# Kernel tuning notes

Hardware: AMD Instinct MI355X
Metric: run time of the kernel (lower is better)

The kernel has to match this reference:

```python
import jax, jax.numpy as jnp
import numpy as np

N = 50000      # nodes (atoms)
E = 1000000    # edges (bonds within cutoff)
L = 3          # num_interactions
G = 512        # graphs in batch
H = 128        # hidden_channels == num_filters
NGAUSS = 50    # num_gaussians
CUTOFF = 10.0
ZMAX = 100     # atomic numbers, < num_embeddings=120
LOG2 = float(np.log(2.0))


def ssp(x):
    # ShiftedSoftplus: softplus(x) - log(2)
    return jax.nn.softplus(x) - LOG2


def setup_inputs() -> dict:
    key = jax.random.key(0)
    ks = jax.random.split(key, 16)

    def w(k, shape, fan_in):
        return jax.random.normal(k, shape, jnp.float32) / np.sqrt(fan_in)

    z = jax.random.randint(ks[0], (N,), 1, ZMAX)
    edge_src = jax.random.randint(ks[1], (E,), 0, N)
    edge_dst = jax.random.randint(ks[2], (E,), 0, N)
    batch = jnp.sort(jax.random.randint(ks[3], (N,), 0, G))
    edge_weight = jax.random.uniform(ks[4], (E,), jnp.float32) * CUTOFF  # distances in [0, cutoff)
    edge_attr = jax.random.normal(ks[5], (E, NGAUSS), jnp.float32)       # gaussian-smeared distances
    return {
        'z': z, 'edge_src': edge_src, 'edge_dst': edge_dst, 'batch': batch,
        'num_graphs': G,
        'edge_weight': edge_weight, 'edge_attr': edge_attr,
        'emb': w(ks[6], (120, H), 1.0),
        'mlp_w1': w(ks[7], (L, NGAUSS, H), NGAUSS), 'mlp_b1': jnp.zeros((L, H), jnp.float32),
        'mlp_w2': w(ks[8], (L, H, H), H), 'mlp_b2': jnp.zeros((L, H), jnp.float32),
        'cf_w1': w(ks[9], (L, H, H), H),
        'cf_w2': w(ks[10], (L, H, H), H), 'cf_b2': jnp.zeros((L, H), jnp.float32),
        'lin_w': w(ks[11], (L, H, H), H), 'lin_b': jnp.zeros((L, H), jnp.float32),
        'ro_w1': w(ks[12], (H, 5 * H), H), 'ro_b1': jnp.zeros((5 * H,), jnp.float32),
        'ro_w2': w(ks[13], (5 * H, H), 5 * H), 'ro_b2': jnp.zeros((H,), jnp.float32),
        'ro_w3': w(ks[14], (H, 1), H), 'ro_b3': jnp.zeros((1,), jnp.float32),
    }


def reference(z, edge_src, edge_dst, batch, num_graphs, edge_weight, edge_attr,
              emb, mlp_w1, mlp_b1, mlp_w2, mlp_b2, cf_w1, cf_w2, cf_b2,
              lin_w, lin_b, ro_w1, ro_b1, ro_w2, ro_b2, ro_w3, ro_b3):
    n_nodes = z.shape[0]
    # simple_z=True: h = relu(Embedding(z))
    h = jax.nn.relu(emb[z])                                   # [N, H]
    # cosine cutoff on distances (shared across blocks)
    C = 0.5 * (jnp.cos(edge_weight * jnp.pi / CUTOFF) + 1.0)  # [E]
    for l in range(L):
        # SchNet filter network on edge attributes
        Wf = ssp(edge_attr @ mlp_w1[l] + mlp_b1[l]) @ mlp_w2[l] + mlp_b2[l]
        Wf = Wf * C[:, None]                                  # [E, H]
        x = h @ cf_w1[l]                                      # CFConv.lin1 (no bias)
        msg = x[edge_src] * Wf                                # gather + filter modulation
        agg = jax.ops.segment_sum(msg, edge_dst, num_segments=n_nodes)  # scatter-add
        x = agg @ cf_w2[l] + cf_b2[l]                         # CFConv.lin2
        x = ssp(x) @ lin_w[l] + lin_b[l]                      # act + block linear
        h = h + x                                             # residual from model forward
    # ReadOutLayer
    hh = ssp(h @ ro_w1 + ro_b1)                               # [N, 5H]
    pooled = jax.ops.segment_sum(hh, batch, num_segments=num_graphs)  # segment_csr 'add'
    out = ssp(pooled @ ro_w2 + ro_b2) @ ro_w3 + ro_b3         # [G, 1]
    return out
```

## Files before the change

### kernel.cpp

```cpp
#include <hip/hip_runtime.h>
#include <math.h>

#define N_NODES 50000
#define N_EDGES 1000000
#define LAYERS  3
#define G_GRAPHS 512
#define H 128
#define NG 50
#define PI_F 3.14159265358979323846f
#define LOG2_F 0.6931471805599453f

typedef __attribute__((ext_vector_type(4))) float f32x4;
typedef __attribute__((ext_vector_type(8))) short short8;

__device__ __forceinline__ float ssp(float v) {
    float t = __expf(-fabsf(v));
    return fmaxf(v, 0.0f) + __logf(1.0f + t) - LOG2_F;
}

__device__ __forceinline__ unsigned short f2bf(float f) {
    unsigned u = __float_as_uint(f);
    unsigned r = (u + 0x7fff + ((u >> 16) & 1)) >> 16;
    return (unsigned short)r;
}
__device__ __forceinline__ float bf2f(unsigned short h) {
    return __uint_as_float((unsigned)h << 16);
}

__global__ __launch_bounds__(256) void init_h(const int* __restrict__ z,
                                              const float* __restrict__ emb,
                                              float* __restrict__ h) {
    int idx = blockIdx.x * 256 + threadIdx.x;
    if (idx >= N_NODES * (H / 4)) return;
    int n = idx >> 5;
    int c4 = idx & 31;
    int zv = z[n];
    float4 v = *(const float4*)(emb + (size_t)zv * H + c4 * 4);
    v.x = fmaxf(v.x, 0.f); v.y = fmaxf(v.y, 0.f);
    v.z = fmaxf(v.z, 0.f); v.w = fmaxf(v.w, 0.f);
    *(float4*)(h + (size_t)n * H + c4 * 4) = v;
}

__global__ __launch_bounds__(256) void hist_kernel(const int* __restrict__ edst,
                                                   int* __restrict__ cnt) {
    int e = blockIdx.x * 256 + threadIdx.x;
    if (e < N_EDGES) atomicAdd(&cnt[edst[e]], 1);
}

__global__ __launch_bounds__(1024) void scan_kernel(const int* __restrict__ cnt,
                                                    int* __restrict__ cur) {
    __shared__ int wsum[16];
    __shared__ int carry_s;
    int tid = threadIdx.x;
    int wid = tid >> 6, lane = tid & 63;
    if (tid == 0) carry_s = 0;
    __syncthreads();
    for (int base = 0; base < N_NODES; base += 1024) {
        int i = base + tid;
        int v = (i < N_NODES) ? cnt[i] : 0;
        int s = v;
#pragma unroll
        for (int d = 1; d < 64; d <<= 1) {
            int t = __shfl_up(s, d, 64);
            if (lane >= d) s += t;
        }
        if (lane == 63) wsum[wid] = s;
        __syncthreads();
        if (wid == 0) {
            int ws = (lane < 16) ? wsum[lane] : 0;
#pragma unroll
            for (int d = 1; d < 16; d <<= 1) {
                int t = __shfl_up(ws, d, 64);
                if (lane >= d) ws += t;
            }
            if (lane < 16) wsum[lane] = ws;
        }
        __syncthreads();
        int waveoff = (wid > 0) ? wsum[wid - 1] : 0;
        int carry = carry_s;
        if (i < N_NODES) cur[i] = carry + waveoff + s - v;
        __syncthreads();
        if (tid == 1023) carry_s = carry + wsum[15];
    }
}

__global__ __launch_bounds__(256) void scatter_kernel(const int* __restrict__ edst,
                                                      int* __restrict__ cur,
                                                      int* __restrict__ perm) {
    int e = blockIdx.x * 256 + threadIdx.x;
    if (e < N_EDGES) {
        int p = atomicAdd(&cur[edst[e]], 1);
        perm[p] = e;
    }
}

__global__ __launch_bounds__(256) void prep_idx(const int* __restrict__ perm,
                                                const int* __restrict__ esrc,
                                                const int* __restrict__ edst,
                                                const float* __restrict__ ew,
                                                int* __restrict__ Sp,
                                                int* __restrict__ Dp,
                                                float* __restrict__ Cp) {
    int pos = blockIdx.x * 256 + threadIdx.x;
    if (pos >= N_EDGES) return;
    int ge = perm[pos];
    Sp[pos] = esrc[ge];
    Dp[pos] = edst[ge];
    Cp[pos] = 0.5f * (cosf(ew[ge] * (PI_F / 10.0f)) + 1.0f);
}

__global__ __launch_bounds__(256) void prep_attr(const int* __restrict__ perm,
                                                 const float* __restrict__ eattr,
                                                 unsigned short* __restrict__ pattr) {
    int t = blockIdx.x * 256 + threadIdx.x;
    int pos = t >> 3, kq = t & 7;
    if (pos >= N_EDGES) return;
    int ge = perm[pos];
    int k0 = kq * 8;
    float v[8] = {0.f, 0.f, 0.f, 0.f, 0.f, 0.f, 0.f, 0.f};
    const float* row = eattr + (size_t)ge * NG;
    if (k0 + 8 <= NG) {
#pragma unroll
        for (int q = 0; q < 4; ++q) {
            float2 a = *(const float2*)(row + k0 + 2 * q);
            v[2 * q] = a.x; v[2 * q + 1] = a.y;
        }
    } else if (k0 < NG) {
        float2 a = *(const float2*)(row + k0);
        v[0] = a.x; v[1] = a.y;
    }
    uint4 wv;
    wv.x = (unsigned)f2bf(v[0]) | ((unsigned)f2bf(v[1]) << 16);
    wv.y = (unsigned)f2bf(v[2]) | ((unsigned)f2bf(v[3]) << 16);
    wv.z = (unsigned)f2bf(v[4]) | ((unsigned)f2bf(v[5]) << 16);
    wv.w = (unsigned)f2bf(v[6]) | ((unsigned)f2bf(v[7]) << 16);
    *(uint4*)(pattr + (size_t)pos * 64 + k0) = wv;
}

__global__ __launch_bounds__(256) void conv_w(const float* __restrict__ mlp_w1,
                                              const float* __restrict__ mlp_w2,
                                              unsigned short* __restrict__ w1t,
                                              unsigned short* __restrict__ w2t) {
    int idx = blockIdx.x * 256 + threadIdx.x;
    const int n1 = LAYERS * 128 * 64;
    if (idx < n1) {
        int l = idx / (128 * 64);
        int rem = idx - l * 128 * 64;
        int col = rem >> 6, k = rem & 63;
        float v = (k < NG) ? mlp_w1[(size_t)l * NG * H + (size_t)k * H + col] : 0.f;
        w1t[idx] = f2bf(v);
        return;
    }
    int idx2 = idx - n1;
    if (idx2 < LAYERS * 128 * 128) {
        int l = idx2 / (128 * 128);
        int rem = idx2 - l * 128 * 128;
        int col = rem >> 7, k = rem & 127;
        w2t[idx2] = f2bf(mlp_w2[(size_t)l * H * H + (size_t)k * H + col]);
    }
}

__global__ __launch_bounds__(256) void conv_nodew(const float* __restrict__ src,
                                                  unsigned short* __restrict__ hi,
                                                  unsigned short* __restrict__ lo,
                                                  int ncols) {
    int idx = blockIdx.x * 256 + threadIdx.x;
    if (idx >= ncols * 128) return;
    int col = idx >> 7, k = idx & 127;
    float v = src[(size_t)k * ncols + col];
    unsigned short h16 = f2bf(v);
    hi[idx] = h16;
    lo[idx] = f2bf(v - bf2f(h16));
}

#define F_BIAS 1
#define F_POOL 8

template <int FLAGS>
__global__ __launch_bounds__(256, 4) void node_gemm_mfma(const float* __restrict__ A,
                                                         const unsigned short* __restrict__ BtHi,
                                                         const unsigned short* __restrict__ BtLo,
                                                         const float* __restrict__ bias,
                                                         float* __restrict__ Out,
                                                         const int* __restrict__ batch,
                                                         int nRows, int NC) {
    __shared__ __align__(16) char ldsHi[64 * 256];
    __shared__ __align__(16) char ldsLo[64 * 256];
    int tid = threadIdx.x;
    int rowBase = blockIdx.x * 64;
    int colOff = blockIdx.y * 128;
    int rlim = nRows - rowBase; if (rlim > 64) rlim = 64;

    for (int idx = tid; idx < 64 * 32; idx += 256) {
        int r = idx >> 5, q = idx & 31;
        float4 v = make_float4(0.f, 0.f, 0.f, 0.f);
        if (r < rlim) v = *(const float4*)(A + (size_t)(rowBase + r) * H + q * 4);
        unsigned short h0 = f2bf(v.x), h1 = f2bf(v.y), h2 = f2bf(v.z), h3 = f2bf(v.w);
        unsigned short l0 = f2bf(v.x - bf2f(h0)), l1 = f2bf(v.y - bf2f(h1));
        unsigned short l2 = f2bf(v.z - bf2f(h2)), l3 = f2bf(v.w - bf2f(h3));
        int byte = (r << 8) + (q << 3);
        byte ^= (r & 7) << 4;
        *(uint2*)(ldsHi + byte) = make_uint2((unsigned)h0 | ((unsigned)h1 << 16),
                                             (unsigned)h2 | ((unsigned)h3 << 16));
        *(uint2*)(ldsLo + byte) = make_uint2((unsigned)l0 | ((unsigned)l1 << 16),
                                             (unsigned)l2 | ((unsigned)l3 << 16));
    }
    __syncthreads();

    int w = tid >> 6, lane = tid & 63;
    int lg = lane >> 4, cg = lane & 15;
    int swA = (cg & 7) << 4;

    f32x4 acc[4][2];
#pragma unroll
    for (int n = 0; n < 2; ++n) {
        float b = (FLAGS & F_BIAS) ? bias[colOff + w * 32 + n * 16 + cg] : 0.f;
        f32x4 t = {b, b, b, b};
#pragma unroll
        for (int m = 0; m < 4; ++m) acc[m][n] = t;
    }

#pragma unroll
    for (int kc = 0; kc < 4; ++kc) {
        short8 aHi[4], aLo[4], bHi[2], bLo[2];
#pragma unroll
        for (int m = 0; m < 4; ++m) {
            int byte = ((m * 16 + cg) << 8) + ((kc * 32 + lg * 8) << 1);
            aHi[m] = *(short8*)(ldsHi + (byte ^ swA));
            aLo[m] = *(short8*)(ldsLo + (byte ^ swA));
        }
#pragma unroll
        for (int n = 0; n < 2; ++n) {
            size_t off = (size_t)(colOff + w * 32 + n * 16 + cg) * 128 + kc * 32 + lg * 8;
            bHi[n] = *(const short8*)(BtHi + off);
            bLo[n] = *(const short8*)(BtLo + off);
        }
#pragma unroll
        for (int m = 0; m < 4; ++m)
#pragma unroll
            for (int n = 0; n < 2; ++n) {
                acc[m][n] = __builtin_amdgcn_mfma_f32_16x16x32_bf16(aHi[m], bHi[n], acc[m][n], 0, 0, 0);
                acc[m][n] = __builtin_amdgcn_mfma_f32_16x16x32_bf16(aLo[m], bHi[n], acc[m][n], 0, 0, 0);
                acc[m][n] = __builtin_amdgcn_mfma_f32_16x16x32_bf16(aHi[m], bLo[n], acc[m][n], 0, 0, 0);
            }
    }

    if (FLAGS & F_POOL) {
        int cur = -1;
        float s[2] = {0.f, 0.f};
#pragma unroll
        for (int m = 0; m < 4; ++m) {
#pragma unroll
            for (int i = 0; i < 4; ++i) {
                int row = m * 16 + lg * 4 + i;
                int b = (row < rlim) ? batch[rowBase + row] : -1;
                if (b != cur) {
                    if (cur >= 0) {
#pragma unroll
                        for (int n = 0; n < 2; ++n)
                            unsafeAtomicAdd(Out + (size_t)cur * NC + colOff + w * 32 + n * 16 + cg, s[n]);
                    }
                    cur = b;
                    s[0] = 0.f; s[1] = 0.f;
                }
                if (b >= 0) {
#pragma unroll
                    for (int n = 0; n < 2; ++n) s[n] += ssp(acc[m][n][i]);
                }
            }
        }
        if (cur >= 0) {
#pragma unroll
            for (int n = 0; n < 2; ++n)
                unsafeAtomicAdd(Out + (size_t)cur * NC + colOff + w * 32 + n * 16 + cg, s[n]);
        }
    } else {
#pragma unroll
        for (int m = 0; m < 4; ++m)
#pragma unroll
            for (int i = 0; i < 4; ++i) {
                int row = m * 16 + lg * 4 + i;
                if (row < rlim) {
#pragma unroll
                    for (int n = 0; n < 2; ++n)
                        Out[(size_t)(rowBase + row) * NC + colOff + w * 32 + n * 16 + cg] = acc[m][n][i];
                }
            }
    }
}

__global__ __launch_bounds__(256, 4) void node_gemm2_mfma(const float* __restrict__ Agg,
                                                          const unsigned short* __restrict__ W2hi,
                                                          const unsigned short* __restrict__ W2lo,
                                                          const float* __restrict__ b2,
                                                          const unsigned short* __restrict__ WLhi,
                                                          const unsigned short* __restrict__ WLlo,
                                                          const float* __restrict__ bl,
                                                          float* __restrict__ Hio,
                                                          int nRows) {
    __shared__ __align__(16) char ldsHi[64 * 256];
    __shared__ __align__(16) char ldsLo[64 * 256];
    int tid = threadIdx.x;
    int rowBase = blockIdx.x * 64;
    int rlim = nRows - rowBase; if (rlim > 64) rlim = 64;

    for (int idx = tid; idx < 64 * 32; idx += 256) {
        int r = idx >> 5, q = idx & 31;
        float4 v = make_float4(0.f, 0.f, 0.f, 0.f);
        if (r < rlim) v = *(const float4*)(Agg + (size_t)(rowBase + r) * H + q * 4);
        unsigned short h0 = f2bf(v.x), h1 = f2bf(v.y), h2 = f2bf(v.z), h3 = f2bf(v.w);
        unsigned short l0 = f2bf(v.x - bf2f(h0)), l1 = f2bf(v.y - bf2f(h1));
        unsigned short l2 = f2bf(v.z - bf2f(h2)), l3 = f2bf(v.w - bf2f(h3));
        int byte = (r << 8) + (q << 3);
        byte ^= (r & 7) << 4;
        *(uint2*)(ldsHi + byte) = make_uint2((unsigned)h0 | ((unsigned)h1 << 16),
                                             (unsigned)h2 | ((unsigned)h3 << 16));
        *(uint2*)(ldsLo + byte) = make_uint2((unsigned)l0 | ((unsigned)l1 << 16),
                                             (unsigned)l2 | ((unsigned)l3 << 16));
    }
    __syncthreads();

    int w = tid >> 6, lane = tid & 63;
    int lg = lane >> 4, cg = lane & 15;
    int swA = (cg & 7) << 4;

    f32x4 acc[4][2];
#pragma unroll
    for (int n = 0; n < 2; ++n) {
        float b = b2[w * 32 + n * 16 + cg];
        f32x4 t = {b, b, b, b};
#pragma unroll
        for (int m = 0; m < 4; ++m) acc[m][n] = t;
    }
#pragma unroll
    for (int kc = 0; kc < 4; ++kc) {
        short8 aHi[4], aLo[4], bHi[2], bLo[2];
#pragma unroll
        for (int m = 0; m < 4; ++m) {
            int byte = ((m * 16 + cg) << 8) + ((kc * 32 + lg * 8) << 1);
            aHi[m] = *(short8*)(ldsHi + (byte ^ swA));
            aLo[m] = *(short8*)(ldsLo + (byte ^ swA));
        }
#pragma unroll
        for (int n = 0; n < 2; ++n) {
            size_t off = (size_t)(w * 32 + n * 16 + cg) * 128 + kc * 32 + lg * 8;
            bHi[n] = *(const short8*)(W2hi + off);
            bLo[n] = *(const short8*)(W2lo + off);
        }
#pragma unroll
        for (int m = 0; m < 4; ++m)
#pragma unroll
            for (int n = 0; n < 2; ++n) {
                acc[m][n] = __builtin_amdgcn_mfma_f32_16x16x32_bf16(aHi[m], bHi[n], acc[m][n], 0, 0, 0);
                acc[m][n] = __builtin_amdgcn_mfma_f32_16x16x32_bf16(aLo[m], bHi[n], acc[m][n], 0, 0, 0);
                acc[m][n] = __builtin_amdgcn_mfma_f32_16x16x32_bf16(aHi[m], bLo[n], acc[m][n], 0, 0, 0);
            }
    }
    __syncthreads();

#pragma unroll
    for (int m = 0; m < 4; ++m)
#pragma unroll
        for (int n = 0; n < 2; ++n)
#pragma unroll
            for (int i = 0; i < 4; ++i) {
                int row = m * 16 + lg * 4 + i;
                int col = w * 32 + n * 16 + cg;
                float v = ssp(acc[m][n][i]);
                unsigned short hh = f2bf(v);
                unsigned short ll = f2bf(v - bf2f(hh));
                int byte = (row << 8) + (col << 1);
                byte ^= (row & 7) << 4;
                *(unsigned short*)(ldsHi + byte) = hh;
                *(unsigned short*)(ldsLo + byte) = ll;
            }
    __syncthreads();

    f32x4 acc2[4][2];
#pragma unroll
    for (int n = 0; n < 2; ++n) {
        float b = bl[w * 32 + n * 16 + cg];
        f32x4 t = {b, b, b, b};
#pragma unroll
        for (int m = 0; m < 4; ++m) acc2[m][n] = t;
    }
#pragma unroll
    for (int kc = 0; kc < 4; ++kc) {
        short8 aHi[4], aLo[4], bHi[2], bLo[2];
#pragma unroll
        for (int m = 0; m < 4; ++m) {
            int byte = ((m * 16 + cg) << 8) + ((kc * 32 + lg * 8) << 1);
            aHi[m] = *(short8*)(ldsHi + (byte ^ swA));
            aLo[m] = *(short8*)(ldsLo + (byte ^ swA));
        }
#pragma unroll
        for (int n = 0; n < 2; ++n) {
            size_t off = (size_t)(w * 32 + n * 16 + cg) * 128 + kc * 32 + lg * 8;
            bHi[n] = *(const short8*)(WLhi + off);
            bLo[n] = *(const short8*)(WLlo + off);
        }
#pragma unroll
        for (int m = 0; m < 4; ++m)
#pragma unroll
            for (int n = 0; n < 2; ++n) {
                acc2[m][n] = __builtin_amdgcn_mfma_f32_16x16x32_bf16(aHi[m], bHi[n], acc2[m][n], 0, 0, 0);
                acc2[m][n] = __builtin_amdgcn_mfma_f32_16x16x32_bf16(aLo[m], bHi[n], acc2[m][n], 0, 0, 0);
                acc2[m][n] = __builtin_amdgcn_mfma_f32_16x16x32_bf16(aHi[m], bLo[n], acc2[m][n], 0, 0, 0);
            }
    }

#pragma unroll
    for (int m = 0; m < 4; ++m)
#pragma unroll
        for (int i = 0; i < 4; ++i) {
            int row = m * 16 + lg * 4 + i;
            if (row < rlim) {
#pragma unroll
                for (int n = 0; n < 2; ++n) {
                    float* p = Hio + (size_t)(rowBase + row) * H + w * 32 + n * 16 + cg;
                    *p += acc2[m][n][i];
                }
            }
        }
}

template <bool IDXP, bool ATTRP>
__global__ __launch_bounds__(256, 5) void edge_kernel(
        const unsigned short* __restrict__ pattr,
        const float* __restrict__ eattr,
        const int* __restrict__ perm,
        const int* __restrict__ esrc,
        const int* __restrict__ edst,
        const float* __restrict__ ew,
        const int* __restrict__ Sp,
        const int* __restrict__ Dp,
        const float* __restrict__ Cp,
        const unsigned short* __restrict__ W1t,
        const float* __restrict__ b1,
        const unsigned short* __restrict__ W2t,
        const float* __restrict__ b2,
        const float* __restrict__ x,
        float* __restrict__ agg) {
    __shared__ __align__(16) char lds[28832];
    float* accT = (float*)(lds + 24576);
    int* RunDst = (int*)(lds + 28800);

    int tid = threadIdx.x;
    int e0 = blockIdx.x * 64;
    int w = tid >> 6, lane = tid & 63;

    for (int i = tid; i < 8 * 132; i += 256) accT[i] = 0.f;

    int ge = 0;
    if (!ATTRP || !IDXP) ge = perm[e0 + lane];
    int S, D; float C;
    if (IDXP) {
        S = Sp[e0 + lane]; D = Dp[e0 + lane]; C = Cp[e0 + lane];
    } else {
        S = esrc[ge]; D = edst[ge];
        C = 0.5f * (cosf(ew[ge] * (PI_F / 10.0f)) + 1.0f);
    }
    int prevd = -1, nextd = -1;
    if (e0 > 0)            prevd = IDXP ? Dp[e0 - 1]  : edst[perm[e0 - 1]];
    if (e0 + 64 < N_EDGES) nextd = IDXP ? Dp[e0 + 64] : edst[perm[e0 + 64]];

    if (ATTRP) {
#pragma unroll
        for (int half = 0; half < 2; ++half) {
            int idx2 = lane + half * 64;
            int row = w * 16 + (idx2 >> 3);
            int q = idx2 & 7;
            uint4 v = *(const uint4*)(pattr + (((size_t)(e0 + row)) << 6) + q * 8);
            int byte = (row << 7) + (q << 4);
            byte ^= (row & 7) << 4;
            *(uint4*)(lds + byte) = v;
        }
    } else {
        int row = w * 16 + (lane >> 2);
        int grow = __shfl(ge, row);
        int jbase = (lane & 3) * 8;
#pragma unroll
        for (int j = 0; j < 8; ++j) {
            int k2 = jbase + j;
            float a0 = 0.f, a1 = 0.f;
            if (k2 < 25) {
                float2 t = *(const float2*)(eattr + (size_t)grow * NG + 2 * k2);
                a0 = t.x; a1 = t.y;
            }
            unsigned p = (unsigned)f2bf(a0) | ((unsigned)f2bf(a1) << 16);
            int byte = (row << 7) + (k2 << 2);
            byte ^= (row & 7) << 4;
            *(unsigned*)(lds + byte) = p;
        }
    }

    int lg = lane >> 4, cg = lane & 15;
    int eB = w * 16 + cg;
    int swz = (eB & 7) << 4;
    int le0 = w * 16 + lg * 4;

    f32x4 acc1[8];
#pragma unroll
    for (int mt = 0; mt < 8; ++mt)
        acc1[mt] = *(const f32x4*)(b1 + mt * 16 + lg * 4);
#pragma unroll
    for (int kc = 0; kc < 2; ++kc) {
        int byteB = (eB << 7) + (kc << 6) + (lg << 4);
        short8 bfrag = *(short8*)(lds + (byteB ^ swz));
#pragma unroll
        for (int mt = 0; mt < 8; ++mt) {
            short8 afrag = *(const short8*)(W1t + ((mt * 16 + cg) << 6) + (kc << 5) + (lg << 3));
            acc1[mt] = __builtin_amdgcn_mfma_f32_16x16x32_bf16(afrag, bfrag, acc1[mt], 0, 0, 0);
        }
    }
#pragma unroll
    for (int mt = 0; mt < 8; ++mt) {
        f32x4 v = acc1[mt];
        unsigned p0 = (unsigned)f2bf(ssp(v[0])) | ((unsigned)f2bf(ssp(v[1])) << 16);
        unsigned p1 = (unsigned)f2bf(ssp(v[2])) | ((unsigned)f2bf(ssp(v[3])) << 16);
        int byte = 8192 + (eB << 8) + (mt << 5) + (lg << 3);
        *(uint2*)(lds + (byte ^ swz)) = make_uint2(p0, p1);
    }

    f32x4 acc2[8];
#pragma unroll
    for (int n = 0; n < 8; ++n) {
        float bb = b2[n * 16 + cg];
        f32x4 t = {bb, bb, bb, bb};
        acc2[n] = t;
    }
#pragma unroll
    for (int kc = 0; kc < 4; ++kc) {
        int byteA = 8192 + (eB << 8) + (kc << 6) + (lg << 4);
        short8 afrag = *(short8*)(lds + (byteA ^ swz));
#pragma unroll
        for (int n = 0; n < 8; ++n) {
            short8 bfrag = *(const short8*)(W2t + ((n * 16 + cg) << 7) + (kc << 5) + (lg << 3));
            acc2[n] = __builtin_amdgcn_mfma_f32_16x16x32_bf16(afrag, bfrag, acc2[n], 0, 0, 0);
        }
    }

    float xv[4][8];
#pragma unroll
    for (int i = 0; i < 4; ++i) {
        int sle = __shfl(S, le0 + i);
        const float* xrow = x + (size_t)sle * H + cg;
#pragma unroll
        for (int n = 0; n < 8; ++n) xv[i][n] = xrow[n * 16];
    }

    int dprev = __shfl_up(D, 1, 64);
    int flag = (lane > 0 && D != dprev) ? 1 : 0;
    int rid = flag;
#pragma unroll
    for (int s2 = 1; s2 < 64; s2 <<= 1) {
        int o = __shfl_up(rid, s2, 64);
        if (lane >= s2) rid += o;
    }
    int nruns = __shfl(rid, 63) + 1;
    if (w == 0 && (lane == 0 || flag) && rid < 8) RunDst[rid] = D;

    asm volatile("s_waitcnt lgkmcnt(0)" ::: "memory");
    __builtin_amdgcn_s_barrier();
    asm volatile("" ::: "memory");

    int curR = -1, curD = 0;
    float part[8];
#pragma unroll
    for (int i = 0; i < 4; ++i) {
        int le = le0 + i;
        int r  = __shfl(rid, le);
        int dd = __shfl(D, le);
        float cf = __shfl(C, le);
        float m[8];
#pragma unroll
        for (int n = 0; n < 8; ++n) m[n] = xv[i][n] * acc2[n][i] * cf;
        if (r != curR) {
            if (curR >= 0) {
                if (curR < 8) {
#pragma unroll
                    for (int n = 0; n < 8; ++n)
                        atomicAdd(accT + curR * 132 + n * 16 + cg, part[n]);
                } else {
#pragma unroll
                    for (int n = 0; n < 8; ++n)
                        unsafeAtomicAdd(agg + (size_t)curD * H + n * 16 + cg, part[n]);
                }
            }
            curR = r; curD = dd;
#pragma unroll
            for (int n = 0; n < 8; ++n) part[n] = m[n];
        } else {
#pragma unroll
            for (int n = 0; n < 8; ++n) part[n] += m[n];
        }
    }
    if (curR < 8) {
#pragma unroll
        for (int n = 0; n < 8; ++n)
            atomicAdd(accT + curR * 132 + n * 16 + cg, part[n]);
    } else {
#pragma unroll
        for (int n = 0; n < 8; ++n)
            unsafeAtomicAdd(agg + (size_t)curD * H + n * 16 + cg, part[n]);
    }

    asm volatile("s_waitcnt lgkmcnt(0)" ::: "memory");
    __builtin_amdgcn_s_barrier();
    asm volatile("" ::: "memory");

    int nstore = (nruns < 8) ? nruns : 8;
    for (int idx = tid; idx < nstore * H; idx += 256) {
        int r = idx >> 7, c = idx & 127;
        float v = accT[r * 132 + c];
        int d = RunDst[r];
        bool shared_run = (r == 0 && d == prevd) || (r == nruns - 1 && d == nextd);
        float* p = agg + (size_t)d * H + c;
        if (shared_run) unsafeAtomicAdd(p, v);
        else *p = v;
    }
}

__global__ __launch_bounds__(128) void final_out(const float* __restrict__ pooled,
                                                 const float* __restrict__ ro_w2,
                                                 const float* __restrict__ ro_b2,
                                                 const float* __restrict__ ro_w3,
                                                 const float* __restrict__ ro_b3,
                                                 float* __restrict__ out) {
    int g = blockIdx.x;
    int c = threadIdx.x;
    float acc = ro_b2[c];
    const float* pr = pooled + (size_t)g * (5 * H);
    for (int k = 0; k < 5 * H; ++k) acc = fmaf(pr[k], ro_w2[(size_t)k * H + c], acc);
    float v = ssp(acc) * ro_w3[c];
    __shared__ float red[128];
    red[c] = v;
    __syncthreads();
    for (int s = 64; s > 0; s >>= 1) {
        if (c < s) red[c] += red[c + s];
        __syncthreads();
    }
    if (c == 0) out[g] = red[0] + ro_b3[0];
}

extern "C" void kernel_launch(void* const* d_in, const int* in_sizes, int n_in,
                              void* d_out, int out_size, void* d_ws, size_t ws_size,
                              hipStream_t stream) {
    const int* z     = (const int*)d_in[0];
    const int* esrc  = (const int*)d_in[1];
    const int* edst  = (const int*)d_in[2];
    const int* batch = (const int*)d_in[3];
    const float* ew    = (const float*)d_in[5];
    const float* eattr = (const float*)d_in[6];
    const float* emb   = (const float*)d_in[7];
    const float* mlp_w1 = (const float*)d_in[8];
    const float* mlp_b1 = (const float*)d_in[9];
    const float* mlp_w2 = (const float*)d_in[10];
    const float* mlp_b2 = (const float*)d_in[11];
    const float* cf_w1  = (const float*)d_in[12];
    const float* cf_w2  = (const float*)d_in[13];
    const float* cf_b2  = (const float*)d_in[14];
    const float* lin_w  = (const float*)d_in[15];
    const float* lin_b  = (const float*)d_in[16];
    const float* ro_w1  = (const float*)d_in[17];
    const float* ro_b1  = (const float*)d_in[18];
    const float* ro_w2  = (const float*)d_in[19];
    const float* ro_b2  = (const float*)d_in[20];
    const float* ro_w3  = (const float*)d_in[21];
    const float* ro_b3  = (const float*)d_in[22];
    float* out = (float*)d_out;

    char* wp = (char*)d_ws;
    auto alloc = [&](size_t bytes) {
        char* p = wp;
        wp += (bytes + 255) & ~(size_t)255;
        return p;
    };
    float* h      = (float*)alloc((size_t)N_NODES * H * 4);
    float* x      = (float*)alloc((size_t)N_NODES * H * 4);
    float* agg    = (float*)alloc((size_t)N_NODES * H * 4);
    float* pooled = (float*)alloc((size_t)G_GRAPHS * 5 * H * 4);
    int*   cnt    = (int*)alloc(N_NODES * 4);
    int*   cur    = (int*)alloc(N_NODES * 4);
    int*   perm   = (int*)alloc((size_t)N_EDGES * 4);
    unsigned short* w1t  = (unsigned short*)alloc((size_t)LAYERS * 128 * 64 * 2);
    unsigned short* w2t  = (unsigned short*)alloc((size_t)LAYERS * 128 * 128 * 2);
    unsigned short* nwhi = (unsigned short*)alloc((size_t)(9 * 16384 + 640 * 128) * 2);
    unsigned short* nwlo = (unsigned short*)alloc((size_t)(9 * 16384 + 640 * 128) * 2);
    int*   Sp = (int*)alloc((size_t)N_EDGES * 4);
    int*   Dp = (int*)alloc((size_t)N_EDGES * 4);
    float* Cp = (float*)alloc((size_t)N_EDGES * 4);
    size_t used_idx = (size_t)(wp - (char*)d_ws);
    unsigned short* pattr = (unsigned short*)alloc((size_t)N_EDGES * 64 * 2);
    size_t used_attr = (size_t)(wp - (char*)d_ws);

    bool idxp  = ws_size >= used_idx;
    bool attrp = ws_size >= used_attr;

    init_h<<<(N_NODES * (H / 4) + 255) / 256, 256, 0, stream>>>(z, emb, h);

    conv_w<<<(LAYERS * 128 * 64 + LAYERS * 128 * 128 + 255) / 256, 256, 0, stream>>>(
        mlp_w1, mlp_w2, w1t, w2t);
    for (int l = 0; l < LAYERS; ++l) {
        conv_nodew<<<(128 * 128 + 255) / 256, 256, 0, stream>>>(
            cf_w1 + (size_t)l * H * H, nwhi + (size_t)l * 16384, nwlo + (size_t)l * 16384, 128);
        conv_nodew<<<(128 * 128 + 255) / 256, 256, 0, stream>>>(
            cf_w2 + (size_t)l * H * H, nwhi + (size_t)(3 + l) * 16384, nwlo + (size_t)(3 + l) * 16384, 128);
        conv_nodew<<<(128 * 128 + 255) / 256, 256, 0, stream>>>(
            lin_w + (size_t)l * H * H, nwhi + (size_t)(6 + l) * 16384, nwlo + (size_t)(6 + l) * 16384, 128);
    }
    conv_nodew<<<(640 * 128 + 255) / 256, 256, 0, stream>>>(
        ro_w1, nwhi + (size_t)9 * 16384, nwlo + (size_t)9 * 16384, 640);

    hipMemsetAsync(cnt, 0, N_NODES * sizeof(int), stream);
    hist_kernel<<<(N_EDGES + 255) / 256, 256, 0, stream>>>(edst, cnt);
    scan_kernel<<<1, 1024, 0, stream>>>(cnt, cur);
    scatter_kernel<<<(N_EDGES + 255) / 256, 256, 0, stream>>>(edst, cur, perm);

    if (idxp)
        prep_idx<<<(N_EDGES + 255) / 256, 256, 0, stream>>>(perm, esrc, edst, ew, Sp, Dp, Cp);
    if (attrp)
        prep_attr<<<(N_EDGES * 8 + 255) / 256, 256, 0, stream>>>(perm, eattr, pattr);

    int rowTiles = (N_NODES + 63) / 64;
    for (int l = 0; l < LAYERS; ++l) {
        node_gemm_mfma<0><<<dim3(rowTiles, 1), 256, 0, stream>>>(
            h, nwhi + (size_t)l * 16384, nwlo + (size_t)l * 16384, nullptr, x, nullptr, N_NODES, H);
        hipMemsetAsync(agg, 0, (size_t)N_NODES * H * sizeof(float), stream);
        if (attrp)
            edge_kernel<true, true><<<N_EDGES / 64, 256, 0, stream>>>(
                pattr, eattr, perm, esrc, edst, ew, Sp, Dp, Cp,
                w1t + (size_t)l * 128 * 64, mlp_b1 + (size_t)l * H,
                w2t + (size_t)l * 128 * 128, mlp_b2 + (size_t)l * H, x, agg);
        else if (idxp)
            edge_kernel<true, false><<<N_EDGES / 64, 256, 0, stream>>>(
                pattr, eattr, perm, esrc, edst, ew, Sp, Dp, Cp,
                w1t + (size_t)l * 128 * 64, mlp_b1 + (size_t)l * H,
                w2t + (size_t)l * 128 * 128, mlp_b2 + (size_t)l * H, x, agg);
        else
            edge_kernel<false, false><<<N_EDGES / 64, 256, 0, stream>>>(
                pattr, eattr, perm, esrc, edst, ew, Sp, Dp, Cp,
                w1t + (size_t)l * 128 * 64, mlp_b1 + (size_t)l * H,
                w2t + (size_t)l * 128 * 128, mlp_b2 + (size_t)l * H, x, agg);
        node_gemm2_mfma<<<dim3(rowTiles, 1), 256, 0, stream>>>(
            agg,
            nwhi + (size_t)(3 + l) * 16384, nwlo + (size_t)(3 + l) * 16384, cf_b2 + (size_t)l * H,
            nwhi + (size_t)(6 + l) * 16384, nwlo + (size_t)(6 + l) * 16384, lin_b + (size_t)l * H,
            h, N_NODES);
    }

    hipMemsetAsync(pooled, 0, (size_t)G_GRAPHS * 5 * H * sizeof(float), stream);
    node_gemm_mfma<F_BIAS | F_POOL><<<dim3(rowTiles, 5), 256, 0, stream>>>(
        h, nwhi + (size_t)9 * 16384, nwlo + (size_t)9 * 16384, ro_b1, pooled, batch, N_NODES, 5 * H);
    final_out<<<G_GRAPHS, 128, 0, stream>>>(pooled, ro_w2, ro_b2, ro_w3, ro_b3, out);
}
```

Measured before the change: 2.027 ms.

## Fuse node GEMMs across layers, embedding init, agg zeroing; shrink edge LDS

Several independent changes land together. The embedding lookup and ReLU are folded into the first lin1 GEMM. The next layer's lin1 GEMM is fused into the tail of node_gemm2, which also zeroes agg in place of a separate memset. The weight-conversion launches are merged into one kernel. The edge kernel's filter-network MLP is restructured into two halves to halve its intermediate LDS buffer, cutting LDS use and run capacity so more blocks fit per CU (launch bound raised to 8). This trades extra register pressure and serialisation in node_gemm2, and a smaller run cache in the edge kernel, for fewer launches and less memory traffic.

```diff
diff --git a/kernel.cpp b/kernel.cpp
--- a/kernel.cpp
+++ b/kernel.cpp
@@ -25,20 +25,6 @@
 }
 __device__ __forceinline__ float bf2f(unsigned short h) {
     return __uint_as_float((unsigned)h << 16);
-}
-
-__global__ __launch_bounds__(256) void init_h(const int* __restrict__ z,
-                                              const float* __restrict__ emb,
-                                              float* __restrict__ h) {
-    int idx = blockIdx.x * 256 + threadIdx.x;
-    if (idx >= N_NODES * (H / 4)) return;
-    int n = idx >> 5;
-    int c4 = idx & 31;
-    int zv = z[n];
-    float4 v = *(const float4*)(emb + (size_t)zv * H + c4 * 4);
-    v.x = fmaxf(v.x, 0.f); v.y = fmaxf(v.y, 0.f);
-    v.z = fmaxf(v.z, 0.f); v.w = fmaxf(v.w, 0.f);
-    *(float4*)(h + (size_t)n * H + c4 * 4) = v;
 }
 
 __global__ __launch_bounds__(256) void hist_kernel(const int* __restrict__ edst,
@@ -160,21 +146,37 @@
     }
 }
 
-__global__ __launch_bounds__(256) void conv_nodew(const float* __restrict__ src,
-                                                  unsigned short* __restrict__ hi,
-                                                  unsigned short* __restrict__ lo,
-                                                  int ncols) {
+__global__ __launch_bounds__(256) void conv_nodew_all(const float* __restrict__ cf_w1,
+                                                      const float* __restrict__ cf_w2,
+                                                      const float* __restrict__ lin_w,
+                                                      const float* __restrict__ ro_w1,
+                                                      unsigned short* __restrict__ hi,
+                                                      unsigned short* __restrict__ lo) {
     int idx = blockIdx.x * 256 + threadIdx.x;
-    if (idx >= ncols * 128) return;
-    int col = idx >> 7, k = idx & 127;
-    float v = src[(size_t)k * ncols + col];
+    const int SQ = LAYERS * 128 * 128;
+    float v; int dst;
+    if (idx < 3 * SQ) {
+        int fam = idx / SQ, rem = idx - fam * SQ;
+        int l = rem / 16384, r2 = rem & 16383;
+        int col = r2 >> 7, k = r2 & 127;
+        const float* src = (fam == 0) ? cf_w1 : ((fam == 1) ? cf_w2 : lin_w);
+        v = src[(size_t)l * 16384 + (size_t)k * 128 + col];
+        dst = (fam * 3 + l) * 16384 + r2;
+    } else {
+        int j = idx - 3 * SQ;
+        if (j >= 640 * 128) return;
+        int col = j >> 7, k = j & 127;
+        v = ro_w1[(size_t)k * 640 + col];
+        dst = 3 * SQ + j;
+    }
     unsigned short h16 = f2bf(v);
-    hi[idx] = h16;
-    lo[idx] = f2bf(v - bf2f(h16));
+    hi[dst] = h16;
+    lo[dst] = f2bf(v - bf2f(h16));
 }
 
 #define F_BIAS 1
 #define F_POOL 8
+#define F_EMB  16
 
 template <int FLAGS>
 __global__ __launch_bounds__(256, 4) void node_gemm_mfma(const float* __restrict__ A,
@@ -183,7 +185,10 @@
                                                          const float* __restrict__ bias,
                                                          float* __restrict__ Out,
                                                          const int* __restrict__ batch,
-                                                         int nRows, int NC) {
+                                                         int nRows, int NC,
+                                                         const int* __restrict__ z,
+                                                         const float* __restrict__ emb,
+                                                         float* __restrict__ hOut) {
     __shared__ __align__(16) char ldsHi[64 * 256];
     __shared__ __align__(16) char ldsLo[64 * 256];
     int tid = threadIdx.x;
@@ -194,7 +199,17 @@
     for (int idx = tid; idx < 64 * 32; idx += 256) {
         int r = idx >> 5, q = idx & 31;
         float4 v = make_float4(0.f, 0.f, 0.f, 0.f);
-        if (r < rlim) v = *(const float4*)(A + (size_t)(rowBase + r) * H + q * 4);
+        if (r < rlim) {
+            if (FLAGS & F_EMB) {
+                int zr = z[rowBase + r];
+                v = *(const float4*)(emb + (size_t)zr * H + q * 4);
+                v.x = fmaxf(v.x, 0.f); v.y = fmaxf(v.y, 0.f);
+                v.z = fmaxf(v.z, 0.f); v.w = fmaxf(v.w, 0.f);
+                *(float4*)(hOut + (size_t)(rowBase + r) * H + q * 4) = v;
+            } else {
+                v = *(const float4*)(A + (size_t)(rowBase + r) * H + q * 4);
+            }
+        }
         unsigned short h0 = f2bf(v.x), h1 = f2bf(v.y), h2 = f2bf(v.z), h3 = f2bf(v.w);
         unsigned short l0 = f2bf(v.x - bf2f(h0)), l1 = f2bf(v.y - bf2f(h1));
         unsigned short l2 = f2bf(v.z - bf2f(h2)), l3 = f2bf(v.w - bf2f(h3));
@@ -289,14 +304,18 @@
     }
 }
 
-__global__ __launch_bounds__(256, 4) void node_gemm2_mfma(const float* __restrict__ Agg,
+template <bool XNEXT>
+__global__ __launch_bounds__(256, 4) void node_gemm2_mfma(float* __restrict__ Agg,
                                                           const unsigned short* __restrict__ W2hi,
                                                           const unsigned short* __restrict__ W2lo,
                                                           const float* __restrict__ b2,
                                                           const unsigned short* __restrict__ WLhi,
                                                           const unsigned short* __restrict__ WLlo,
                                                           const float* __restrict__ bl,
+                                                          const unsigned short* __restrict__ W1nhi,
+                                                          const unsigned short* __restrict__ W1nlo,
                                                           float* __restrict__ Hio,
+                                                          float* __restrict__ xout,
                                                           int nRows) {
     __shared__ __align__(16) char ldsHi[64 * 256];
     __shared__ __align__(16) char ldsLo[64 * 256];
@@ -307,7 +326,11 @@
     for (int idx = tid; idx < 64 * 32; idx += 256) {
         int r = idx >> 5, q = idx & 31;
         float4 v = make_float4(0.f, 0.f, 0.f, 0.f);
-        if (r < rlim) v = *(const float4*)(Agg + (size_t)(rowBase + r) * H + q * 4);
+        if (r < rlim) {
+            float* p = Agg + (size_t)(rowBase + r) * H + q * 4;
+            v = *(float4*)p;
+            *(float4*)p = make_float4(0.f, 0.f, 0.f, 0.f);
+        }
         unsigned short h0 = f2bf(v.x), h1 = f2bf(v.y), h2 = f2bf(v.z), h3 = f2bf(v.w);
         unsigned short l0 = f2bf(v.x - bf2f(h0)), l1 = f2bf(v.y - bf2f(h1));
         unsigned short l2 = f2bf(v.z - bf2f(h2)), l3 = f2bf(v.w - bf2f(h3));
@@ -409,23 +432,93 @@
             }
     }
 
-#pragma unroll
-    for (int m = 0; m < 4; ++m)
-#pragma unroll
-        for (int i = 0; i < 4; ++i) {
-            int row = m * 16 + lg * 4 + i;
-            if (row < rlim) {
+    if (XNEXT) {
+        __syncthreads();
+#pragma unroll
+        for (int m = 0; m < 4; ++m)
+#pragma unroll
+            for (int n = 0; n < 2; ++n)
+#pragma unroll
+                for (int i = 0; i < 4; ++i) {
+                    int row = m * 16 + lg * 4 + i;
+                    int col = w * 32 + n * 16 + cg;
+                    float hnew = 0.f;
+                    if (row < rlim) {
+                        float* p = Hio + (size_t)(rowBase + row) * H + col;
+                        hnew = *p + acc2[m][n][i];
+                        *p = hnew;
+                    }
+                    unsigned short hh = f2bf(hnew);
+                    unsigned short ll = f2bf(hnew - bf2f(hh));
+                    int byte = (row << 8) + (col << 1);
+                    byte ^= (row & 7) << 4;
+                    *(unsigned short*)(ldsHi + byte) = hh;
+                    *(unsigned short*)(ldsLo + byte) = ll;
+                }
+        __syncthreads();
+
+        f32x4 acc3[4][2];
+#pragma unroll
+        for (int n = 0; n < 2; ++n) {
+            f32x4 t = {0.f, 0.f, 0.f, 0.f};
+#pragma unroll
+            for (int m = 0; m < 4; ++m) acc3[m][n] = t;
+        }
+#pragma unroll
+        for (int kc = 0; kc < 4; ++kc) {
+            short8 aHi[4], aLo[4], bHi[2], bLo[2];
+#pragma unroll
+            for (int m = 0; m < 4; ++m) {
+                int byte = ((m * 16 + cg) << 8) + ((kc * 32 + lg * 8) << 1);
+                aHi[m] = *(short8*)(ldsHi + (byte ^ swA));
+                aLo[m] = *(short8*)(ldsLo + (byte ^ swA));
+            }
+#pragma unroll
+            for (int n = 0; n < 2; ++n) {
+                size_t off = (size_t)(w * 32 + n * 16 + cg) * 128 + kc * 32 + lg * 8;
+                bHi[n] = *(const short8*)(W1nhi + off);
+                bLo[n] = *(const short8*)(W1nlo + off);
+            }
+#pragma unroll
+            for (int m = 0; m < 4; ++m)
 #pragma unroll
                 for (int n = 0; n < 2; ++n) {
-                    float* p = Hio + (size_t)(rowBase + row) * H + w * 32 + n * 16 + cg;
-                    *p += acc2[m][n][i];
+                    acc3[m][n] = __builtin_amdgcn_mfma_f32_16x16x32_bf16(aHi[m], bHi[n], acc3[m][n], 0, 0, 0);
+                    acc3[m][n] = __builtin_amdgcn_mfma_f32_16x16x32_bf16(aLo[m], bHi[n], acc3[m][n], 0, 0, 0);
+                    acc3[m][n] = __builtin_amdgcn_mfma_f32_16x16x32_bf16(aHi[m], bLo[n], acc3[m][n], 0, 0, 0);
                 }
-            }
-        }
-}
-
+        }
+#pragma unroll
+        for (int m = 0; m < 4; ++m)
+#pragma unroll
+            for (int i = 0; i < 4; ++i) {
+                int row = m * 16 + lg * 4 + i;
+                if (row < rlim) {
+#pragma unroll
+                    for (int n = 0; n < 2; ++n)
+                        xout[(size_t)(rowBase + row) * H + w * 32 + n * 16 + cg] = acc3[m][n][i];
+                }
+            }
+    } else {
+#pragma unroll
+        for (int m = 0; m < 4; ++m)
+#pragma unroll
+            for (int i = 0; i < 4; ++i) {
+                int row = m * 16 + lg * 4 + i;
+                if (row < rlim) {
+#pragma unroll
+                    for (int n = 0; n < 2; ++n) {
+                        float* p = Hio + (size_t)(rowBase + row) * H + w * 32 + n * 16 + cg;
+                        *p += acc2[m][n][i];
+                    }
+                }
+            }
+    }
+}
+
+#define RUNCAP 7
 template <bool IDXP, bool ATTRP>
-__global__ __launch_bounds__(256, 5) void edge_kernel(
+__global__ __launch_bounds__(256, 8) void edge_kernel(
         const unsigned short* __restrict__ pattr,
         const float* __restrict__ eattr,
         const int* __restrict__ perm,
@@ -441,15 +534,15 @@
         const float* __restrict__ b2,
         const float* __restrict__ x,
         float* __restrict__ agg) {
-    __shared__ __align__(16) char lds[28832];
-    float* accT = (float*)(lds + 24576);
-    int* RunDst = (int*)(lds + 28800);
+    __shared__ __align__(16) char lds[20112];
+    float* accT = (float*)(lds + 16384);
+    int* RunDst = (int*)(lds + 20080);
 
     int tid = threadIdx.x;
     int e0 = blockIdx.x * 64;
     int w = tid >> 6, lane = tid & 63;
 
-    for (int i = tid; i < 8 * 132; i += 256) accT[i] = 0.f;
+    for (int i = tid; i < RUNCAP * 132; i += 256) accT[i] = 0.f;
 
     int ge = 0;
     if (!ATTRP || !IDXP) ge = perm[e0 + lane];
@@ -499,27 +592,11 @@
     int swz = (eB & 7) << 4;
     int le0 = w * 16 + lg * 4;
 
-    f32x4 acc1[8];
-#pragma unroll
-    for (int mt = 0; mt < 8; ++mt)
-        acc1[mt] = *(const f32x4*)(b1 + mt * 16 + lg * 4);
+    short8 bfragA[2];
 #pragma unroll
     for (int kc = 0; kc < 2; ++kc) {
         int byteB = (eB << 7) + (kc << 6) + (lg << 4);
-        short8 bfrag = *(short8*)(lds + (byteB ^ swz));
-#pragma unroll
-        for (int mt = 0; mt < 8; ++mt) {
-            short8 afrag = *(const short8*)(W1t + ((mt * 16 + cg) << 6) + (kc << 5) + (lg << 3));
-            acc1[mt] = __builtin_amdgcn_mfma_f32_16x16x32_bf16(afrag, bfrag, acc1[mt], 0, 0, 0);
-        }
-    }
-#pragma unroll
-    for (int mt = 0; mt < 8; ++mt) {
-        f32x4 v = acc1[mt];
-        unsigned p0 = (unsigned)f2bf(ssp(v[0])) | ((unsigned)f2bf(ssp(v[1])) << 16);
-        unsigned p1 = (unsigned)f2bf(ssp(v[2])) | ((unsigned)f2bf(ssp(v[3])) << 16);
-        int byte = 8192 + (eB << 8) + (mt << 5) + (lg << 3);
-        *(uint2*)(lds + (byte ^ swz)) = make_uint2(p0, p1);
+        bfragA[kc] = *(short8*)(lds + (byteB ^ swz));
     }
 
     f32x4 acc2[8];
@@ -529,14 +606,37 @@
         f32x4 t = {bb, bb, bb, bb};
         acc2[n] = t;
     }
-#pragma unroll
-    for (int kc = 0; kc < 4; ++kc) {
-        int byteA = 8192 + (eB << 8) + (kc << 6) + (lg << 4);
-        short8 afrag = *(short8*)(lds + (byteA ^ swz));
-#pragma unroll
-        for (int n = 0; n < 8; ++n) {
-            short8 bfrag = *(const short8*)(W2t + ((n * 16 + cg) << 7) + (kc << 5) + (lg << 3));
-            acc2[n] = __builtin_amdgcn_mfma_f32_16x16x32_bf16(afrag, bfrag, acc2[n], 0, 0, 0);
+
+#pragma unroll
+    for (int p = 0; p < 2; ++p) {
+        f32x4 acc1[4];
+#pragma unroll
+        for (int mtL = 0; mtL < 4; ++mtL)
+            acc1[mtL] = *(const f32x4*)(b1 + (p * 4 + mtL) * 16 + lg * 4);
+#pragma unroll
+        for (int kc = 0; kc < 2; ++kc)
+#pragma unroll
+            for (int mtL = 0; mtL < 4; ++mtL) {
+                short8 afrag = *(const short8*)(W1t + (((p * 4 + mtL) * 16 + cg) << 6) + (kc << 5) + (lg << 3));
+                acc1[mtL] = __builtin_amdgcn_mfma_f32_16x16x32_bf16(afrag, bfragA[kc], acc1[mtL], 0, 0, 0);
+            }
+#pragma unroll
+        for (int mtL = 0; mtL < 4; ++mtL) {
+            f32x4 v = acc1[mtL];
+            unsigned p0 = (unsigned)f2bf(ssp(v[0])) | ((unsigned)f2bf(ssp(v[1])) << 16);
+            unsigned p1 = (unsigned)f2bf(ssp(v[2])) | ((unsigned)f2bf(ssp(v[3])) << 16);
+            int byte = 8192 + (eB << 7) + (mtL << 5) + (lg << 3);
+            *(uint2*)(lds + (byte ^ swz)) = make_uint2(p0, p1);
+        }
+#pragma unroll
+        for (int kcL = 0; kcL < 2; ++kcL) {
+            int byteA = 8192 + (eB << 7) + (kcL << 6) + (lg << 4);
+            short8 afrag2 = *(short8*)(lds + (byteA ^ swz));
+#pragma unroll
+            for (int n = 0; n < 8; ++n) {
+                short8 bfrag2 = *(const short8*)(W2t + ((n * 16 + cg) << 7) + (((p << 1) + kcL) << 5) + (lg << 3));
+                acc2[n] = __builtin_amdgcn_mfma_f32_16x16x32_bf16(afrag2, bfrag2, acc2[n], 0, 0, 0);
+            }
         }
     }
 
@@ -558,7 +658,7 @@
         if (lane >= s2) rid += o;
     }
     int nruns = __shfl(rid, 63) + 1;
-    if (w == 0 && (lane == 0 || flag) && rid < 8) RunDst[rid] = D;
+    if (w == 0 && (lane == 0 || flag) && rid < RUNCAP) RunDst[rid] = D;
 
     asm volatile("s_waitcnt lgkmcnt(0)" ::: "memory");
     __builtin_amdgcn_s_barrier();
@@ -577,7 +677,7 @@
         for (int n = 0; n < 8; ++n) m[n] = xv[i][n] * acc2[n][i] * cf;
         if (r != curR) {
             if (curR >= 0) {
-                if (curR < 8) {
+                if (curR < RUNCAP) {
 #pragma unroll
                     for (int n = 0; n < 8; ++n)
                         atomicAdd(accT + curR * 132 + n * 16 + cg, part[n]);
@@ -595,7 +695,7 @@
             for (int n = 0; n < 8; ++n) part[n] += m[n];
         }
     }
-    if (curR < 8) {
+    if (curR < RUNCAP) {
 #pragma unroll
         for (int n = 0; n < 8; ++n)
             atomicAdd(accT + curR * 132 + n * 16 + cg, part[n]);
@@ -609,7 +709,7 @@
     __builtin_amdgcn_s_barrier();
     asm volatile("" ::: "memory");
 
-    int nstore = (nruns < 8) ? nruns : 8;
+    int nstore = (nruns < RUNCAP) ? nruns : RUNCAP;
     for (int idx = tid; idx < nstore * H; idx += 256) {
         int r = idx >> 7, c = idx & 127;
         float v = accT[r * 132 + c];
@@ -697,20 +797,10 @@
     bool idxp  = ws_size >= used_idx;
     bool attrp = ws_size >= used_attr;
 
-    init_h<<<(N_NODES * (H / 4) + 255) / 256, 256, 0, stream>>>(z, emb, h);
-
     conv_w<<<(LAYERS * 128 * 64 + LAYERS * 128 * 128 + 255) / 256, 256, 0, stream>>>(
         mlp_w1, mlp_w2, w1t, w2t);
-    for (int l = 0; l < LAYERS; ++l) {
-        conv_nodew<<<(128 * 128 + 255) / 256, 256, 0, stream>>>(
-            cf_w1 + (size_t)l * H * H, nwhi + (size_t)l * 16384, nwlo + (size_t)l * 16384, 128);
-        conv_nodew<<<(128 * 128 + 255) / 256, 256, 0, stream>>>(
-            cf_w2 + (size_t)l * H * H, nwhi + (size_t)(3 + l) * 16384, nwlo + (size_t)(3 + l) * 16384, 128);
-        conv_nodew<<<(128 * 128 + 255) / 256, 256, 0, stream>>>(
-            lin_w + (size_t)l * H * H, nwhi + (size_t)(6 + l) * 16384, nwlo + (size_t)(6 + l) * 16384, 128);
-    }
-    conv_nodew<<<(640 * 128 + 255) / 256, 256, 0, stream>>>(
-        ro_w1, nwhi + (size_t)9 * 16384, nwlo + (size_t)9 * 16384, 640);
+    conv_nodew_all<<<(3 * LAYERS * 128 * 128 + 640 * 128 + 255) / 256, 256, 0, stream>>>(
+        cf_w1, cf_w2, lin_w, ro_w1, nwhi, nwlo);
 
     hipMemsetAsync(cnt, 0, N_NODES * sizeof(int), stream);
     hist_kernel<<<(N_EDGES + 255) / 256, 256, 0, stream>>>(edst, cnt);
@@ -723,10 +813,12 @@
         prep_attr<<<(N_EDGES * 8 + 255) / 256, 256, 0, stream>>>(perm, eattr, pattr);
 
     int rowTiles = (N_NODES + 63) / 64;
+
+    node_gemm_mfma<F_EMB><<<dim3(rowTiles, 1), 256, 0, stream>>>(
+        nullptr, nwhi, nwlo, nullptr, x, nullptr, N_NODES, H, z, emb, h);
+    hipMemsetAsync(agg, 0, (size_t)N_NODES * H * sizeof(float), stream);
+
     for (int l = 0; l < LAYERS; ++l) {
-        node_gemm_mfma<0><<<dim3(rowTiles, 1), 256, 0, stream>>>(
-            h, nwhi + (size_t)l * 16384, nwlo + (size_t)l * 16384, nullptr, x, nullptr, N_NODES, H);
-        hipMemsetAsync(agg, 0, (size_t)N_NODES * H * sizeof(float), stream);
         if (attrp)
             edge_kernel<true, true><<<N_EDGES / 64, 256, 0, stream>>>(
                 pattr, eattr, perm, esrc, edst, ew, Sp, Dp, Cp,
@@ -742,15 +834,26 @@
                 pattr, eattr, perm, esrc, edst, ew, Sp, Dp, Cp,
                 w1t + (size_t)l * 128 * 64, mlp_b1 + (size_t)l * H,
                 w2t + (size_t)l * 128 * 128, mlp_b2 + (size_t)l * H, x, agg);
-        node_gemm2_mfma<<<dim3(rowTiles, 1), 256, 0, stream>>>(
-            agg,
-            nwhi + (size_t)(3 + l) * 16384, nwlo + (size_t)(3 + l) * 16384, cf_b2 + (size_t)l * H,
-            nwhi + (size_t)(6 + l) * 16384, nwlo + (size_t)(6 + l) * 16384, lin_b + (size_t)l * H,
-            h, N_NODES);
+        if (l < LAYERS - 1) {
+            node_gemm2_mfma<true><<<dim3(rowTiles, 1), 256, 0, stream>>>(
+                agg,
+                nwhi + (size_t)(3 + l) * 16384, nwlo + (size_t)(3 + l) * 16384, cf_b2 + (size_t)l * H,
+                nwhi + (size_t)(6 + l) * 16384, nwlo + (size_t)(6 + l) * 16384, lin_b + (size_t)l * H,
+                nwhi + (size_t)(l + 1) * 16384, nwlo + (size_t)(l + 1) * 16384,
+                h, x, N_NODES);
+        } else {
+            node_gemm2_mfma<false><<<dim3(rowTiles, 1), 256, 0, stream>>>(
+                agg,
+                nwhi + (size_t)(3 + l) * 16384, nwlo + (size_t)(3 + l) * 16384, cf_b2 + (size_t)l * H,
+                nwhi + (size_t)(6 + l) * 16384, nwlo + (size_t)(6 + l) * 16384, lin_b + (size_t)l * H,
+                nullptr, nullptr,
+                h, nullptr, N_NODES);
+        }
     }
 
     hipMemsetAsync(pooled, 0, (size_t)G_GRAPHS * 5 * H * sizeof(float), stream);
     node_gemm_mfma<F_BIAS | F_POOL><<<dim3(rowTiles, 5), 256, 0, stream>>>(
-        h, nwhi + (size_t)9 * 16384, nwlo + (size_t)9 * 16384, ro_b1, pooled, batch, N_NODES, 5 * H);
+        h, nwhi + (size_t)9 * 16384, nwlo + (size_t)9 * 16384, ro_b1, pooled, batch, N_NODES, 5 * H,
+        nullptr, nullptr, nullptr);
     final_out<<<G_GRAPHS, 128, 0, stream>>>(pooled, ro_w2, ro_b2, ro_w3, ro_b3, out);
 }
```

Result: slower. 3.546 ms (+74.9%).
